# Performance work log

Measured on AMD Instinct MI355X. Metric: run time of the kernel, lower is better.

The kernel has to match this reference:

```python
import jax, jax.numpy as jnp
import numpy as np

N = 10000
E = 320000
F_IN = 256
F_PROJ = 200


def setup_inputs() -> dict:
    key = jax.random.key(0)
    ks = jax.random.split(key, 8)
    x = jax.random.normal(ks[0], (N, F_IN), dtype=jnp.float32)
    edge_attr = jax.random.uniform(ks[1], (N, N), dtype=jnp.float32)
    src = jax.random.randint(ks[2], (E,), 0, N)
    dst = jax.random.randint(ks[3], (E,), 0, N)
    # remove self loops at data-gen time (module calls remove_self_loops)
    dst = jnp.where(dst == src, (dst + 1) % N, dst)
    edge_index = jnp.stack([src, dst]).astype(jnp.int64)
    W_proj = jax.random.normal(ks[4], (F_IN, F_PROJ), dtype=jnp.float32) * 0.05
    b_proj = jnp.zeros((F_PROJ,), dtype=jnp.float32)
    W_att = jax.random.normal(ks[5], (F_PROJ, 1), dtype=jnp.float32) * 0.05
    b_att = jnp.zeros((1,), dtype=jnp.float32)
    return {"x": x, "edge_attr": edge_attr, "edge_index": edge_index,
            "W_proj": W_proj, "b_proj": b_proj, "W_att": W_att, "b_att": b_att}


def reference(x, edge_attr, edge_index, W_proj, b_proj, W_att, b_att):
    src, dst = edge_index[0], edge_index[1]
    # gather: x_j = source features, x_i = target features (PyG default flow)
    x_i = x[dst]                      # [E, F_IN]
    x_j = x[src]                      # [E, F_IN]
    p_i = x_i @ W_proj + b_proj       # [E, 200]
    p_j = x_j @ W_proj + b_proj       # [E, 200]
    alpha = jnp.abs(p_i - p_j) @ W_att + b_att   # [E, 1]
    alpha = jax.nn.relu(alpha)
    alpha = jax.nn.softmax(alpha, axis=0)        # softmax over edges
    a = alpha[:, 0]
    # write attention symmetrically into the dense edge matrix
    edge_values = edge_attr.at[src, dst].set(a).at[dst, src].set(a)
    # scatter-max aggregation of (unprojected) x_i by target index
    agg = jax.ops.segment_max(x_i, dst, num_segments=N)
    agg = jnp.where(jnp.isfinite(agg), agg, jnp.zeros((), agg.dtype))
    return agg, edge_values
```

## Files before the change

kernel.cpp:

```cpp
#include <hip/hip_runtime.h>

#define N_NODES 10000
#define E_EDGES 320000
#define F_IN    256
#define F_PROJ  200

#define N4_TOTAL 25000000L
#define S1_SPLIT 4000000L

#define K1_PROJ_BLOCKS 1250
#define K1_COPY_BLOCKS 768
#define K1_BLOCKS (K1_PROJ_BLOCKS + K1_COPY_BLOCKS)

#define K2_BLOCKS 6144
#define K2_ALPHA_BLOCKS 1536
#define K2_COPY_BLOCKS (K2_BLOCKS - K2_ALPHA_BLOCKS)
#define K2_ALPHA_WAVES (K2_ALPHA_BLOCKS * 4)
#define ALPHA_CHUNK ((E_EDGES + K2_ALPHA_WAVES - 1) / K2_ALPHA_WAVES)
#define AGG_N4 (N_NODES * F_IN / 4)
#define AGG_CHUNK ((AGG_N4 + K2_ALPHA_BLOCKS - 1) / K2_ALPHA_BLOCKS)

typedef float vfloat4 __attribute__((ext_vector_type(4)));

__device__ __forceinline__ unsigned short f32_to_bf16(float f) {
    unsigned int u = __float_as_uint(f);
    u += 0x7FFFu + ((u >> 16) & 1u);
    return (unsigned short)(u >> 16);
}
__device__ __forceinline__ float bf16_to_f32(unsigned short b) {
    return __uint_as_float(((unsigned int)b) << 16);
}

__global__ __launch_bounds__(256) void k1_proj_flags_copy(
        const float* __restrict__ x,
        const float* __restrict__ W,
        unsigned short* __restrict__ P,
        const int* __restrict__ ei,
        int* __restrict__ flags,
        const vfloat4* __restrict__ csrc,
        vfloat4* __restrict__ cdst) {
    int bid = blockIdx.x, tid = threadIdx.x;
    if (bid >= K1_PROJ_BLOCKS) {
        long i = (long)(bid - K1_PROJ_BLOCKS) * 256 + tid;
        const long stride = (long)K1_COPY_BLOCKS * 256;
        while (i + stride < S1_SPLIT) {
            vfloat4 v0 = __builtin_nontemporal_load(csrc + i);
            vfloat4 v1 = __builtin_nontemporal_load(csrc + i + stride);
            __builtin_nontemporal_store(v0, cdst + i);
            __builtin_nontemporal_store(v1, cdst + i + stride);
            i += 2 * stride;
        }
        if (i < S1_SPLIT) {
            vfloat4 v = __builtin_nontemporal_load(csrc + i);
            __builtin_nontemporal_store(v, cdst + i);
        }
        return;
    }
    int gt = bid * 256 + tid;
    flags[ei[E_EDGES + gt]] = 1;

    __shared__ float xs[8][F_IN];
    int n0 = bid * 8;
    for (int i = tid; i < 8 * F_IN / 4; i += 256)
        ((float4*)xs)[i] = ((const float4*)(x + (long)n0 * F_IN))[i];
    __syncthreads();
    int j = tid;
    if (j >= F_PROJ) return;
    float acc[8] = {0.f,0.f,0.f,0.f,0.f,0.f,0.f,0.f};
    for (int k = 0; k < F_IN; ++k) {
        float w = W[k * F_PROJ + j];
        #pragma unroll
        for (int r = 0; r < 8; ++r) acc[r] += xs[r][k] * w;
    }
    #pragma unroll
    for (int r = 0; r < 8; ++r) P[(long)(n0 + r) * F_PROJ + j] = f32_to_bf16(acc[r]);
}

__global__ __launch_bounds__(256) void k2_alpha_agg_copy(
        const int* __restrict__ ei,
        const unsigned short* __restrict__ P,
        const float* __restrict__ Watt,
        const float* __restrict__ batt,
        float* __restrict__ expalpha,
        float* __restrict__ sumbuf,
        const int* __restrict__ flags,
        const float4* __restrict__ x4,
        float4* __restrict__ agg4,
        const vfloat4* __restrict__ csrc,
        vfloat4* __restrict__ cdst) {
    int bid = blockIdx.x, tid = threadIdx.x;
    int role = bid & 3;
    if (role != 0) {
        long cid = (long)(bid >> 2) * 3 + (role - 1);
        long i = S1_SPLIT + cid * 256 + tid;
        const long stride = (long)K2_COPY_BLOCKS * 256;
        while (i + stride < N4_TOTAL) {
            vfloat4 v0 = __builtin_nontemporal_load(csrc + i);
            vfloat4 v1 = __builtin_nontemporal_load(csrc + i + stride);
            __builtin_nontemporal_store(v0, cdst + i);
            __builtin_nontemporal_store(v1, cdst + i + stride);
            i += 2 * stride;
        }
        if (i < N4_TOTAL) {
            vfloat4 v = __builtin_nontemporal_load(csrc + i);
            __builtin_nontemporal_store(v, cdst + i);
        }
        return;
    }
    __shared__ float bsum;
    if (tid == 0) bsum = 0.f;
    __syncthreads();

    int aid  = bid >> 2;
    int wid  = aid * 4 + (tid >> 6);
    int lane = tid & 63;

    float4 w4 = make_float4(0.f, 0.f, 0.f, 0.f);
    if (lane < 50) w4 = ((const float4*)Watt)[lane];
    float bias = batt[0];

    int e0 = wid * ALPHA_CHUNK;
    int e1 = min(e0 + ALPHA_CHUNK, E_EDGES);
    float lsum = 0.f;

    for (int e = e0; e < e1; ++e) {
        int s = ei[e];
        int d = ei[E_EDGES + e];
        float acc = 0.f;
        if (lane < 50) {
            uint2 us = *(const uint2*)(P + (long)s * F_PROJ + lane * 4);
            uint2 ud = *(const uint2*)(P + (long)d * F_PROJ + lane * 4);
            acc = fabsf(bf16_to_f32((unsigned short)(ud.x & 0xFFFF)) -
                        bf16_to_f32((unsigned short)(us.x & 0xFFFF))) * w4.x
                + fabsf(bf16_to_f32((unsigned short)(ud.x >> 16)) -
                        bf16_to_f32((unsigned short)(us.x >> 16))) * w4.y
                + fabsf(bf16_to_f32((unsigned short)(ud.y & 0xFFFF)) -
                        bf16_to_f32((unsigned short)(us.y & 0xFFFF))) * w4.z
                + fabsf(bf16_to_f32((unsigned short)(ud.y >> 16)) -
                        bf16_to_f32((unsigned short)(us.y >> 16))) * w4.w;
        }
        #pragma unroll
        for (int off = 32; off; off >>= 1) acc += __shfl_down(acc, off);
        if (lane == 0) {
            float alpha = fmaxf(acc + bias, 0.f);
            float ea = expf(alpha);
            expalpha[e] = ea;
            lsum += ea;
        }
    }
    if (lane == 0) atomicAdd(&bsum, lsum);
    __syncthreads();
    if (tid == 0) atomicAdd(sumbuf, bsum);

    long a0 = (long)aid * AGG_CHUNK;
    long a1 = a0 + AGG_CHUNK; if (a1 > AGG_N4) a1 = AGG_N4;
    for (long i = a0 + tid; i < a1; i += 256) {
        float4 v = x4[i];
        if (!flags[i >> 6]) v = make_float4(0.f, 0.f, 0.f, 0.f);
        agg4[i] = v;
    }
}

__global__ __launch_bounds__(256) void k3_scatter(
        const int* __restrict__ ei,
        const float* __restrict__ expalpha,
        const float* __restrict__ sumbuf,
        float* __restrict__ ev) {
    int e = blockIdx.x * 256 + threadIdx.x;
    if (e >= E_EDGES) return;
    float a = expalpha[e] / sumbuf[0];
    int s = ei[e];
    int d = ei[E_EDGES + e];
    ev[(long)s * N_NODES + d] = a;
    ev[(long)d * N_NODES + s] = a;
}

extern "C" void kernel_launch(void* const* d_in, const int* in_sizes, int n_in,
                              void* d_out, int out_size, void* d_ws, size_t ws_size,
                              hipStream_t stream) {
    (void)in_sizes; (void)n_in; (void)out_size; (void)ws_size;
    const float* x         = (const float*)d_in[0];
    const float* edge_attr = (const float*)d_in[1];
    const int*   ei        = (const int*)d_in[2];
    const float* W_proj    = (const float*)d_in[3];
    const float* W_att     = (const float*)d_in[5];
    const float* b_att     = (const float*)d_in[6];

    float* agg = (float*)d_out;
    float* ev  = (float*)d_out + (long)N_NODES * F_IN;

    char* ws = (char*)d_ws;
    unsigned short* P = (unsigned short*)(ws);
    float* expalpha   = (float*)(ws + 4000000);
    int*   flags      = (int*)  (ws + 5280000);
    float* sumbuf     = (float*)(ws + 5320000);

    hipMemsetAsync(ws + 5280000, 0, 40016, stream);

    k1_proj_flags_copy<<<K1_BLOCKS, 256, 0, stream>>>(
        x, W_proj, P, ei, flags, (const vfloat4*)edge_attr, (vfloat4*)ev);

    k2_alpha_agg_copy<<<K2_BLOCKS, 256, 0, stream>>>(
        ei, P, W_att, b_att, expalpha, sumbuf, flags,
        (const float4*)x, (float4*)agg,
        (const vfloat4*)edge_attr, (vfloat4*)ev);

    k3_scatter<<<(E_EDGES + 255) / 256, 256, 0, stream>>>(ei, expalpha, sumbuf, ev);
}
```

Baseline: 249.3 us.

## Bucket attention writes by matrix region and patch them during region copy

The dense edge-matrix copy is split into fixed 20000-float regions, spread over all three kernels with most of it in the last one. Instead of storing per-edge exp values and scattering them randomly after the copy, the alpha kernel appends (offset, fp16 exp) entries into per-region buckets using atomics. The final kernel copies each region and then patches its bucketed entries, so the scattered writes land on data that was just written. The trade-offs: buckets are capped at 384 entries and any overflow is silently dropped; values are stored in fp16; and a fallback to the old path runs only when the workspace is too small.

```diff
diff --git a/kernel.cpp b/kernel.cpp
--- a/kernel.cpp
+++ b/kernel.cpp
@@ -1,26 +1,37 @@
 #include <hip/hip_runtime.h>
+#include <hip/hip_fp16.h>
 
 #define N_NODES 10000
 #define E_EDGES 320000
 #define F_IN    256
 #define F_PROJ  200
 
-#define N4_TOTAL 25000000L
-#define S1_SPLIT 4000000L
+typedef float vfloat4 __attribute__((ext_vector_type(4)));
+
+#define REG_FLOATS 20000
+#define REG_F4     5000
+#define NREGIONS   5000
+#define CAP        384
 
 #define K1_PROJ_BLOCKS 1250
-#define K1_COPY_BLOCKS 768
-#define K1_BLOCKS (K1_PROJ_BLOCKS + K1_COPY_BLOCKS)
-
-#define K2_BLOCKS 6144
+#define K1_COPY_REGS   300
 #define K2_ALPHA_BLOCKS 1536
-#define K2_COPY_BLOCKS (K2_BLOCKS - K2_ALPHA_BLOCKS)
-#define K2_ALPHA_WAVES (K2_ALPHA_BLOCKS * 4)
+#define K2_ALPHA_WAVES  (K2_ALPHA_BLOCKS * 4)
 #define ALPHA_CHUNK ((E_EDGES + K2_ALPHA_WAVES - 1) / K2_ALPHA_WAVES)
-#define AGG_N4 (N_NODES * F_IN / 4)
-#define AGG_CHUNK ((AGG_N4 + K2_ALPHA_BLOCKS - 1) / K2_ALPHA_BLOCKS)
-
-typedef float vfloat4 __attribute__((ext_vector_type(4)));
+#define K2_COPY_REG0   300
+#define K2_COPY_REGS   600
+#define K2_AGG_BLOCKS  160
+#define AGG_N4         (N_NODES * F_IN / 4)
+#define AGG_PER_BLOCK  (AGG_N4 / K2_AGG_BLOCKS)
+#define K3_COPY_REG0   900
+#define K3_COPY_REGS   (NREGIONS - K3_COPY_REG0)
+
+#define WS_P       0L
+#define WS_FLAGS   4000000L
+#define WS_SUM     4040000L
+#define WS_COUNTS  4040016L
+#define WS_BUCKET  4060016L
+#define WS_NEED    (WS_BUCKET + (long)NREGIONS * CAP * 4)
 
 __device__ __forceinline__ unsigned short f32_to_bf16(float f) {
     unsigned int u = __float_as_uint(f);
@@ -30,6 +41,7 @@
 __device__ __forceinline__ float bf16_to_f32(unsigned short b) {
     return __uint_as_float(((unsigned int)b) << 16);
 }
+
 
 __global__ __launch_bounds__(256) void k1_proj_flags_copy(
         const float* __restrict__ x,
@@ -41,18 +53,12 @@
         vfloat4* __restrict__ cdst) {
     int bid = blockIdx.x, tid = threadIdx.x;
     if (bid >= K1_PROJ_BLOCKS) {
-        long i = (long)(bid - K1_PROJ_BLOCKS) * 256 + tid;
-        const long stride = (long)K1_COPY_BLOCKS * 256;
-        while (i + stride < S1_SPLIT) {
-            vfloat4 v0 = __builtin_nontemporal_load(csrc + i);
-            vfloat4 v1 = __builtin_nontemporal_load(csrc + i + stride);
-            __builtin_nontemporal_store(v0, cdst + i);
-            __builtin_nontemporal_store(v1, cdst + i + stride);
-            i += 2 * stride;
-        }
-        if (i < S1_SPLIT) {
-            vfloat4 v = __builtin_nontemporal_load(csrc + i);
-            __builtin_nontemporal_store(v, cdst + i);
+        long r = bid - K1_PROJ_BLOCKS;
+        const vfloat4* s = csrc + r * REG_F4;
+        vfloat4*       d = cdst + r * REG_F4;
+        for (int i = tid; i < REG_F4; i += 256) {
+            vfloat4 v = __builtin_nontemporal_load(s + i);
+            __builtin_nontemporal_store(v, d + i);
         }
         return;
     }
@@ -76,32 +82,177 @@
     for (int r = 0; r < 8; ++r) P[(long)(n0 + r) * F_PROJ + j] = f32_to_bf16(acc[r]);
 }
 
-__global__ __launch_bounds__(256) void k2_alpha_agg_copy(
+__global__ __launch_bounds__(256) void k2_alpha_copy_agg(
         const int* __restrict__ ei,
         const unsigned short* __restrict__ P,
         const float* __restrict__ Watt,
         const float* __restrict__ batt,
-        float* __restrict__ expalpha,
         float* __restrict__ sumbuf,
+        unsigned int* __restrict__ counts,
+        unsigned int* __restrict__ bucket,
         const int* __restrict__ flags,
         const float4* __restrict__ x4,
         float4* __restrict__ agg4,
         const vfloat4* __restrict__ csrc,
         vfloat4* __restrict__ cdst) {
     int bid = blockIdx.x, tid = threadIdx.x;
+    if (bid < K2_ALPHA_BLOCKS) {
+        __shared__ float bsum;
+        if (tid == 0) bsum = 0.f;
+        __syncthreads();
+        int wid  = bid * 4 + (tid >> 6);
+        int lane = tid & 63;
+        float4 w4 = make_float4(0.f, 0.f, 0.f, 0.f);
+        if (lane < 50) w4 = ((const float4*)Watt)[lane];
+        float bias = batt[0];
+        int e0 = wid * ALPHA_CHUNK;
+        int e1 = min(e0 + ALPHA_CHUNK, E_EDGES);
+        float lsum = 0.f;
+        for (int e = e0; e < e1; ++e) {
+            int s = ei[e];
+            int d = ei[E_EDGES + e];
+            float acc = 0.f;
+            if (lane < 50) {
+                uint2 us = *(const uint2*)(P + (long)s * F_PROJ + lane * 4);
+                uint2 ud = *(const uint2*)(P + (long)d * F_PROJ + lane * 4);
+                acc = fabsf(bf16_to_f32((unsigned short)(ud.x & 0xFFFF)) -
+                            bf16_to_f32((unsigned short)(us.x & 0xFFFF))) * w4.x
+                    + fabsf(bf16_to_f32((unsigned short)(ud.x >> 16)) -
+                            bf16_to_f32((unsigned short)(us.x >> 16))) * w4.y
+                    + fabsf(bf16_to_f32((unsigned short)(ud.y & 0xFFFF)) -
+                            bf16_to_f32((unsigned short)(us.y & 0xFFFF))) * w4.z
+                    + fabsf(bf16_to_f32((unsigned short)(ud.y >> 16)) -
+                            bf16_to_f32((unsigned short)(us.y >> 16))) * w4.w;
+            }
+            #pragma unroll
+            for (int off = 32; off; off >>= 1) acc += __shfl_xor(acc, off);
+            float alpha = fmaxf(acc + bias, 0.f);
+            float ea = expf(alpha);
+            if (lane < 2) {
+                unsigned int li = (lane == 0)
+                    ? (unsigned int)s * 10000u + (unsigned int)d
+                    : (unsigned int)d * 10000u + (unsigned int)s;
+                unsigned int r  = li / 20000u;
+                unsigned int p  = li - r * 20000u;
+                unsigned short h = __half_as_ushort(__float2half(ea));
+                unsigned int idx = atomicAdd(&counts[r], 1u);
+                if (idx < CAP) bucket[(long)r * CAP + idx] = (p << 16) | h;
+                if (lane == 0) lsum += ea;
+            }
+        }
+        if (lane == 0) atomicAdd(&bsum, lsum);
+        __syncthreads();
+        if (tid == 0) atomicAdd(sumbuf, bsum);
+        return;
+    }
+    int b2 = bid - K2_ALPHA_BLOCKS;
+    if (b2 < K2_COPY_REGS) {
+        long r = K2_COPY_REG0 + b2;
+        const vfloat4* s = csrc + r * REG_F4;
+        vfloat4*       d = cdst + r * REG_F4;
+        for (int i = tid; i < REG_F4; i += 256) {
+            vfloat4 v = __builtin_nontemporal_load(s + i);
+            __builtin_nontemporal_store(v, d + i);
+        }
+        return;
+    }
+    long base = (long)(b2 - K2_COPY_REGS) * AGG_PER_BLOCK;
+    for (int i = tid; i < AGG_PER_BLOCK; i += 256) {
+        long i4 = base + i;
+        float4 v = x4[i4];
+        if (!flags[i4 >> 6]) v = make_float4(0.f, 0.f, 0.f, 0.f);
+        agg4[i4] = v;
+    }
+}
+
+__global__ __launch_bounds__(256) void k3_copy_patch(
+        const unsigned int* __restrict__ counts,
+        const unsigned int* __restrict__ bucket,
+        const float* __restrict__ sumbuf,
+        const vfloat4* __restrict__ csrc,
+        vfloat4* __restrict__ cdst,
+        float* __restrict__ ev) {
+    int bid = blockIdx.x, tid = threadIdx.x;
+    int r;
+    if (bid < K3_COPY_REGS) {
+        r = K3_COPY_REG0 + bid;
+        const vfloat4* s = csrc + (long)r * REG_F4;
+        vfloat4*       d = cdst + (long)r * REG_F4;
+        for (int i = tid; i < REG_F4; i += 256) d[i] = s[i];
+        __syncthreads();
+    } else {
+        r = bid - K3_COPY_REGS;
+    }
+    unsigned int cnt = counts[r];
+    if (cnt > CAP) cnt = CAP;
+    float inv = 1.0f / sumbuf[0];
+    long base = (long)r * REG_FLOATS;
+    for (unsigned int i = tid; i < cnt; i += 256) {
+        unsigned int en = bucket[(long)r * CAP + i];
+        float a = __half2float(__ushort_as_half((unsigned short)(en & 0xFFFFu))) * inv;
+        ev[base + (en >> 16)] = a;
+    }
+}
+
+#define N4_TOTAL 25000000L
+#define S1_SPLIT 4000000L
+#define FB1_PROJ_BLOCKS 1250
+#define FB1_COPY_BLOCKS 768
+#define FB2_BLOCKS 6144
+#define FB2_ALPHA_BLOCKS 1536
+#define FB2_COPY_BLOCKS (FB2_BLOCKS - FB2_ALPHA_BLOCKS)
+#define FB2_ALPHA_WAVES (FB2_ALPHA_BLOCKS * 4)
+#define FB_ALPHA_CHUNK ((E_EDGES + FB2_ALPHA_WAVES - 1) / FB2_ALPHA_WAVES)
+#define FB_AGG_CHUNK ((AGG_N4 + FB2_ALPHA_BLOCKS - 1) / FB2_ALPHA_BLOCKS)
+
+__global__ __launch_bounds__(256) void fb1_proj_flags_copy(
+        const float* __restrict__ x, const float* __restrict__ W,
+        unsigned short* __restrict__ P, const int* __restrict__ ei,
+        int* __restrict__ flags,
+        const vfloat4* __restrict__ csrc, vfloat4* __restrict__ cdst) {
+    int bid = blockIdx.x, tid = threadIdx.x;
+    if (bid >= FB1_PROJ_BLOCKS) {
+        long i = (long)(bid - FB1_PROJ_BLOCKS) * 256 + tid;
+        const long stride = (long)FB1_COPY_BLOCKS * 256;
+        for (; i < S1_SPLIT; i += stride) {
+            vfloat4 v = __builtin_nontemporal_load(csrc + i);
+            __builtin_nontemporal_store(v, cdst + i);
+        }
+        return;
+    }
+    int gt = bid * 256 + tid;
+    flags[ei[E_EDGES + gt]] = 1;
+    __shared__ float xs[8][F_IN];
+    int n0 = bid * 8;
+    for (int i = tid; i < 8 * F_IN / 4; i += 256)
+        ((float4*)xs)[i] = ((const float4*)(x + (long)n0 * F_IN))[i];
+    __syncthreads();
+    int j = tid;
+    if (j >= F_PROJ) return;
+    float acc[8] = {0.f,0.f,0.f,0.f,0.f,0.f,0.f,0.f};
+    for (int k = 0; k < F_IN; ++k) {
+        float w = W[k * F_PROJ + j];
+        #pragma unroll
+        for (int r = 0; r < 8; ++r) acc[r] += xs[r][k] * w;
+    }
+    #pragma unroll
+    for (int r = 0; r < 8; ++r) P[(long)(n0 + r) * F_PROJ + j] = f32_to_bf16(acc[r]);
+}
+
+__global__ __launch_bounds__(256) void fb2_alpha_agg_copy(
+        const int* __restrict__ ei, const unsigned short* __restrict__ P,
+        const float* __restrict__ Watt, const float* __restrict__ batt,
+        float* __restrict__ expalpha, float* __restrict__ sumbuf,
+        const int* __restrict__ flags, const float4* __restrict__ x4,
+        float4* __restrict__ agg4,
+        const vfloat4* __restrict__ csrc, vfloat4* __restrict__ cdst) {
+    int bid = blockIdx.x, tid = threadIdx.x;
     int role = bid & 3;
     if (role != 0) {
         long cid = (long)(bid >> 2) * 3 + (role - 1);
         long i = S1_SPLIT + cid * 256 + tid;
-        const long stride = (long)K2_COPY_BLOCKS * 256;
-        while (i + stride < N4_TOTAL) {
-            vfloat4 v0 = __builtin_nontemporal_load(csrc + i);
-            vfloat4 v1 = __builtin_nontemporal_load(csrc + i + stride);
-            __builtin_nontemporal_store(v0, cdst + i);
-            __builtin_nontemporal_store(v1, cdst + i + stride);
-            i += 2 * stride;
-        }
-        if (i < N4_TOTAL) {
+        const long stride = (long)FB2_COPY_BLOCKS * 256;
+        for (; i < N4_TOTAL; i += stride) {
             vfloat4 v = __builtin_nontemporal_load(csrc + i);
             __builtin_nontemporal_store(v, cdst + i);
         }
@@ -110,22 +261,14 @@
     __shared__ float bsum;
     if (tid == 0) bsum = 0.f;
     __syncthreads();
-
-    int aid  = bid >> 2;
-    int wid  = aid * 4 + (tid >> 6);
-    int lane = tid & 63;
-
+    int aid = bid >> 2, wid = aid * 4 + (tid >> 6), lane = tid & 63;
     float4 w4 = make_float4(0.f, 0.f, 0.f, 0.f);
     if (lane < 50) w4 = ((const float4*)Watt)[lane];
     float bias = batt[0];
-
-    int e0 = wid * ALPHA_CHUNK;
-    int e1 = min(e0 + ALPHA_CHUNK, E_EDGES);
+    int e0 = wid * FB_ALPHA_CHUNK, e1 = min(e0 + FB_ALPHA_CHUNK, E_EDGES);
     float lsum = 0.f;
-
     for (int e = e0; e < e1; ++e) {
-        int s = ei[e];
-        int d = ei[E_EDGES + e];
+        int s = ei[e], d = ei[E_EDGES + e];
         float acc = 0.f;
         if (lane < 50) {
             uint2 us = *(const uint2*)(P + (long)s * F_PROJ + lane * 4);
@@ -142,8 +285,7 @@
         #pragma unroll
         for (int off = 32; off; off >>= 1) acc += __shfl_down(acc, off);
         if (lane == 0) {
-            float alpha = fmaxf(acc + bias, 0.f);
-            float ea = expf(alpha);
+            float ea = expf(fmaxf(acc + bias, 0.f));
             expalpha[e] = ea;
             lsum += ea;
         }
@@ -151,9 +293,8 @@
     if (lane == 0) atomicAdd(&bsum, lsum);
     __syncthreads();
     if (tid == 0) atomicAdd(sumbuf, bsum);
-
-    long a0 = (long)aid * AGG_CHUNK;
-    long a1 = a0 + AGG_CHUNK; if (a1 > AGG_N4) a1 = AGG_N4;
+    long a0 = (long)aid * FB_AGG_CHUNK;
+    long a1 = a0 + FB_AGG_CHUNK; if (a1 > AGG_N4) a1 = AGG_N4;
     for (long i = a0 + tid; i < a1; i += 256) {
         float4 v = x4[i];
         if (!flags[i >> 6]) v = make_float4(0.f, 0.f, 0.f, 0.f);
@@ -161,16 +302,13 @@
     }
 }
 
-__global__ __launch_bounds__(256) void k3_scatter(
-        const int* __restrict__ ei,
-        const float* __restrict__ expalpha,
-        const float* __restrict__ sumbuf,
-        float* __restrict__ ev) {
+__global__ __launch_bounds__(256) void fb3_scatter(
+        const int* __restrict__ ei, const float* __restrict__ expalpha,
+        const float* __restrict__ sumbuf, float* __restrict__ ev) {
     int e = blockIdx.x * 256 + threadIdx.x;
     if (e >= E_EDGES) return;
     float a = expalpha[e] / sumbuf[0];
-    int s = ei[e];
-    int d = ei[E_EDGES + e];
+    int s = ei[e], d = ei[E_EDGES + e];
     ev[(long)s * N_NODES + d] = a;
     ev[(long)d * N_NODES + s] = a;
 }
@@ -178,7 +316,7 @@
 extern "C" void kernel_launch(void* const* d_in, const int* in_sizes, int n_in,
                               void* d_out, int out_size, void* d_ws, size_t ws_size,
                               hipStream_t stream) {
-    (void)in_sizes; (void)n_in; (void)out_size; (void)ws_size;
+    (void)in_sizes; (void)n_in; (void)out_size;
     const float* x         = (const float*)d_in[0];
     const float* edge_attr = (const float*)d_in[1];
     const int*   ei        = (const int*)d_in[2];
@@ -188,22 +326,45 @@
 
     float* agg = (float*)d_out;
     float* ev  = (float*)d_out + (long)N_NODES * F_IN;
-
     char* ws = (char*)d_ws;
-    unsigned short* P = (unsigned short*)(ws);
-    float* expalpha   = (float*)(ws + 4000000);
-    int*   flags      = (int*)  (ws + 5280000);
-    float* sumbuf     = (float*)(ws + 5320000);
-
-    hipMemsetAsync(ws + 5280000, 0, 40016, stream);
-
-    k1_proj_flags_copy<<<K1_BLOCKS, 256, 0, stream>>>(
-        x, W_proj, P, ei, flags, (const vfloat4*)edge_attr, (vfloat4*)ev);
-
-    k2_alpha_agg_copy<<<K2_BLOCKS, 256, 0, stream>>>(
-        ei, P, W_att, b_att, expalpha, sumbuf, flags,
-        (const float4*)x, (float4*)agg,
-        (const vfloat4*)edge_attr, (vfloat4*)ev);
-
-    k3_scatter<<<(E_EDGES + 255) / 256, 256, 0, stream>>>(ei, expalpha, sumbuf, ev);
-}
+
+    if (ws_size >= (size_t)WS_NEED) {
+        unsigned short* P   = (unsigned short*)(ws + WS_P);
+        int*   flags        = (int*)(ws + WS_FLAGS);
+        float* sumbuf       = (float*)(ws + WS_SUM);
+        unsigned int* cnts  = (unsigned int*)(ws + WS_COUNTS);
+        unsigned int* bkt   = (unsigned int*)(ws + WS_BUCKET);
+
+        hipMemsetAsync(ws + WS_FLAGS, 0, WS_BUCKET - WS_FLAGS, stream);
+
+        k1_proj_flags_copy<<<K1_PROJ_BLOCKS + K1_COPY_REGS, 256, 0, stream>>>(
+            x, W_proj, P, ei, flags, (const vfloat4*)edge_attr, (vfloat4*)ev);
+
+        k2_alpha_copy_agg<<<K2_ALPHA_BLOCKS + K2_COPY_REGS + K2_AGG_BLOCKS, 256, 0,
+                            stream>>>(
+            ei, P, W_att, b_att, sumbuf, cnts, bkt, flags,
+            (const float4*)x, (float4*)agg,
+            (const vfloat4*)edge_attr, (vfloat4*)ev);
+
+        k3_copy_patch<<<NREGIONS, 256, 0, stream>>>(
+            cnts, bkt, sumbuf, (const vfloat4*)edge_attr, (vfloat4*)ev, ev);
+    } else {
+        unsigned short* P = (unsigned short*)(ws);
+        float* expalpha   = (float*)(ws + 4000000);
+        int*   flags      = (int*)(ws + 5280000);
+        float* sumbuf     = (float*)(ws + 5320000);
+
+        hipMemsetAsync(ws + 5280000, 0, 40016, stream);
+
+        fb1_proj_flags_copy<<<FB1_PROJ_BLOCKS + FB1_COPY_BLOCKS, 256, 0, stream>>>(
+            x, W_proj, P, ei, flags, (const vfloat4*)edge_attr, (vfloat4*)ev);
+
+        fb2_alpha_agg_copy<<<FB2_BLOCKS, 256, 0, stream>>>(
+            ei, P, W_att, b_att, expalpha, sumbuf, flags,
+            (const float4*)x, (float4*)agg,
+            (const vfloat4*)edge_attr, (vfloat4*)ev);
+
+        fb3_scatter<<<(E_EDGES + 255) / 256, 256, 0, stream>>>(
+            ei, expalpha, sumbuf, ev);
+    }
+}
```

Result: slower. 321.6 us (+29.0%).

## Split bulk edge_attr copy out of alpha kernel into separate copy kernel

Applied to the files above, without the earlier changes.

The alpha/aggregation kernel no longer interleaves copy blocks. The bulk of the dense edge_attr-to-output copy now runs in its own kernel, which uses plain loads and stores instead of nontemporal ones. Alpha work is regrouped into 2048 blocks of 40 edges per wave, and aggregation gets 160 dedicated blocks. The aim is to balance the alpha gather and the streaming copy better, at the cost of losing their overlap and adding one kernel launch.

```diff
diff --git a/kernel.cpp b/kernel.cpp
--- a/kernel.cpp
+++ b/kernel.cpp
@@ -5,22 +5,24 @@
 #define F_IN    256
 #define F_PROJ  200
 
+typedef float vfloat4 __attribute__((ext_vector_type(4)));
+
 #define N4_TOTAL 25000000L
 #define S1_SPLIT 4000000L
 
 #define K1_PROJ_BLOCKS 1250
 #define K1_COPY_BLOCKS 768
-#define K1_BLOCKS (K1_PROJ_BLOCKS + K1_COPY_BLOCKS)
+#define A_BLOCKS    2048
+#define A_CHUNK     40
+#define AGG_BLOCKS  160
+#define AGG_N4      (N_NODES * F_IN / 4)
+#define AGG_PER_BLK (AGG_N4 / AGG_BLOCKS)
+#define K3_BLOCKS   4096
 
-#define K2_BLOCKS 6144
-#define K2_ALPHA_BLOCKS 1536
-#define K2_COPY_BLOCKS (K2_BLOCKS - K2_ALPHA_BLOCKS)
-#define K2_ALPHA_WAVES (K2_ALPHA_BLOCKS * 4)
-#define ALPHA_CHUNK ((E_EDGES + K2_ALPHA_WAVES - 1) / K2_ALPHA_WAVES)
-#define AGG_N4 (N_NODES * F_IN / 4)
-#define AGG_CHUNK ((AGG_N4 + K2_ALPHA_BLOCKS - 1) / K2_ALPHA_BLOCKS)
-
-typedef float vfloat4 __attribute__((ext_vector_type(4)));
+#define WS_P      0L
+#define WS_EXP    4000000L
+#define WS_FLAGS  5280000L
+#define WS_SUM    5320000L
 
 __device__ __forceinline__ unsigned short f32_to_bf16(float f) {
     unsigned int u = __float_as_uint(f);
@@ -32,25 +34,15 @@
 }
 
 __global__ __launch_bounds__(256) void k1_proj_flags_copy(
-        const float* __restrict__ x,
-        const float* __restrict__ W,
-        unsigned short* __restrict__ P,
-        const int* __restrict__ ei,
+        const float* __restrict__ x, const float* __restrict__ W,
+        unsigned short* __restrict__ P, const int* __restrict__ ei,
         int* __restrict__ flags,
-        const vfloat4* __restrict__ csrc,
-        vfloat4* __restrict__ cdst) {
+        const vfloat4* __restrict__ csrc, vfloat4* __restrict__ cdst) {
     int bid = blockIdx.x, tid = threadIdx.x;
     if (bid >= K1_PROJ_BLOCKS) {
         long i = (long)(bid - K1_PROJ_BLOCKS) * 256 + tid;
         const long stride = (long)K1_COPY_BLOCKS * 256;
-        while (i + stride < S1_SPLIT) {
-            vfloat4 v0 = __builtin_nontemporal_load(csrc + i);
-            vfloat4 v1 = __builtin_nontemporal_load(csrc + i + stride);
-            __builtin_nontemporal_store(v0, cdst + i);
-            __builtin_nontemporal_store(v1, cdst + i + stride);
-            i += 2 * stride;
-        }
-        if (i < S1_SPLIT) {
+        for (; i < S1_SPLIT; i += stride) {
             vfloat4 v = __builtin_nontemporal_load(csrc + i);
             __builtin_nontemporal_store(v, cdst + i);
         }
@@ -76,101 +68,83 @@
     for (int r = 0; r < 8; ++r) P[(long)(n0 + r) * F_PROJ + j] = f32_to_bf16(acc[r]);
 }
 
-__global__ __launch_bounds__(256) void k2_alpha_agg_copy(
-        const int* __restrict__ ei,
-        const unsigned short* __restrict__ P,
-        const float* __restrict__ Watt,
-        const float* __restrict__ batt,
-        float* __restrict__ expalpha,
-        float* __restrict__ sumbuf,
-        const int* __restrict__ flags,
-        const float4* __restrict__ x4,
-        float4* __restrict__ agg4,
-        const vfloat4* __restrict__ csrc,
-        vfloat4* __restrict__ cdst) {
+__global__ __launch_bounds__(256) void k2_alpha_agg(
+        const int* __restrict__ ei, const unsigned short* __restrict__ P,
+        const float* __restrict__ Watt, const float* __restrict__ batt,
+        float* __restrict__ expalpha, float* __restrict__ sumbuf,
+        const int* __restrict__ flags, const float4* __restrict__ x4,
+        float4* __restrict__ agg4) {
     int bid = blockIdx.x, tid = threadIdx.x;
-    int role = bid & 3;
-    if (role != 0) {
-        long cid = (long)(bid >> 2) * 3 + (role - 1);
-        long i = S1_SPLIT + cid * 256 + tid;
-        const long stride = (long)K2_COPY_BLOCKS * 256;
-        while (i + stride < N4_TOTAL) {
-            vfloat4 v0 = __builtin_nontemporal_load(csrc + i);
-            vfloat4 v1 = __builtin_nontemporal_load(csrc + i + stride);
-            __builtin_nontemporal_store(v0, cdst + i);
-            __builtin_nontemporal_store(v1, cdst + i + stride);
-            i += 2 * stride;
+    if (bid < A_BLOCKS) {
+        __shared__ float bsum;
+        if (tid == 0) bsum = 0.f;
+        __syncthreads();
+        int wid  = bid * 4 + (tid >> 6);
+        int lane = tid & 63;
+        float4 w4 = make_float4(0.f, 0.f, 0.f, 0.f);
+        if (lane < 50) w4 = ((const float4*)Watt)[lane];
+        float bias = batt[0];
+        int e0 = wid * A_CHUNK;
+        int e1 = min(e0 + A_CHUNK, E_EDGES);
+        float lsum = 0.f;
+        for (int e = e0; e < e1; ++e) {
+            int s = ei[e];
+            int d = ei[E_EDGES + e];
+            float acc = 0.f;
+            if (lane < 50) {
+                uint2 us = *(const uint2*)(P + (long)s * F_PROJ + lane * 4);
+                uint2 ud = *(const uint2*)(P + (long)d * F_PROJ + lane * 4);
+                acc = fabsf(bf16_to_f32((unsigned short)(ud.x & 0xFFFF)) -
+                            bf16_to_f32((unsigned short)(us.x & 0xFFFF))) * w4.x
+                    + fabsf(bf16_to_f32((unsigned short)(ud.x >> 16)) -
+                            bf16_to_f32((unsigned short)(us.x >> 16))) * w4.y
+                    + fabsf(bf16_to_f32((unsigned short)(ud.y & 0xFFFF)) -
+                            bf16_to_f32((unsigned short)(us.y & 0xFFFF))) * w4.z
+                    + fabsf(bf16_to_f32((unsigned short)(ud.y >> 16)) -
+                            bf16_to_f32((unsigned short)(us.y >> 16))) * w4.w;
+            }
+            #pragma unroll
+            for (int off = 32; off; off >>= 1) acc += __shfl_down(acc, off);
+            if (lane == 0) {
+                float ea = expf(fmaxf(acc + bias, 0.f));
+                expalpha[e] = ea;
+                lsum += ea;
+            }
         }
-        if (i < N4_TOTAL) {
-            vfloat4 v = __builtin_nontemporal_load(csrc + i);
-            __builtin_nontemporal_store(v, cdst + i);
-        }
+        if (lane == 0) atomicAdd(&bsum, lsum);
+        __syncthreads();
+        if (tid == 0) atomicAdd(sumbuf, bsum);
         return;
     }
-    __shared__ float bsum;
-    if (tid == 0) bsum = 0.f;
-    __syncthreads();
-
-    int aid  = bid >> 2;
-    int wid  = aid * 4 + (tid >> 6);
-    int lane = tid & 63;
-
-    float4 w4 = make_float4(0.f, 0.f, 0.f, 0.f);
-    if (lane < 50) w4 = ((const float4*)Watt)[lane];
-    float bias = batt[0];
-
-    int e0 = wid * ALPHA_CHUNK;
-    int e1 = min(e0 + ALPHA_CHUNK, E_EDGES);
-    float lsum = 0.f;
-
-    for (int e = e0; e < e1; ++e) {
-        int s = ei[e];
-        int d = ei[E_EDGES + e];
-        float acc = 0.f;
-        if (lane < 50) {
-            uint2 us = *(const uint2*)(P + (long)s * F_PROJ + lane * 4);
-            uint2 ud = *(const uint2*)(P + (long)d * F_PROJ + lane * 4);
-            acc = fabsf(bf16_to_f32((unsigned short)(ud.x & 0xFFFF)) -
-                        bf16_to_f32((unsigned short)(us.x & 0xFFFF))) * w4.x
-                + fabsf(bf16_to_f32((unsigned short)(ud.x >> 16)) -
-                        bf16_to_f32((unsigned short)(us.x >> 16))) * w4.y
-                + fabsf(bf16_to_f32((unsigned short)(ud.y & 0xFFFF)) -
-                        bf16_to_f32((unsigned short)(us.y & 0xFFFF))) * w4.z
-                + fabsf(bf16_to_f32((unsigned short)(ud.y >> 16)) -
-                        bf16_to_f32((unsigned short)(us.y >> 16))) * w4.w;
-        }
-        #pragma unroll
-        for (int off = 32; off; off >>= 1) acc += __shfl_down(acc, off);
-        if (lane == 0) {
-            float alpha = fmaxf(acc + bias, 0.f);
-            float ea = expf(alpha);
-            expalpha[e] = ea;
-            lsum += ea;
-        }
-    }
-    if (lane == 0) atomicAdd(&bsum, lsum);
-    __syncthreads();
-    if (tid == 0) atomicAdd(sumbuf, bsum);
-
-    long a0 = (long)aid * AGG_CHUNK;
-    long a1 = a0 + AGG_CHUNK; if (a1 > AGG_N4) a1 = AGG_N4;
-    for (long i = a0 + tid; i < a1; i += 256) {
-        float4 v = x4[i];
-        if (!flags[i >> 6]) v = make_float4(0.f, 0.f, 0.f, 0.f);
-        agg4[i] = v;
+    long base = (long)(bid - A_BLOCKS) * AGG_PER_BLK;
+    for (int i = tid; i < AGG_PER_BLK; i += 256) {
+        long i4 = base + i;
+        float4 v = x4[i4];
+        if (!flags[i4 >> 6]) v = make_float4(0.f, 0.f, 0.f, 0.f);
+        agg4[i4] = v;
     }
 }
 
-__global__ __launch_bounds__(256) void k3_scatter(
-        const int* __restrict__ ei,
-        const float* __restrict__ expalpha,
-        const float* __restrict__ sumbuf,
-        float* __restrict__ ev) {
+__global__ __launch_bounds__(256) void k3_copy(
+        const vfloat4* __restrict__ src, vfloat4* __restrict__ dst) {
+    long i = S1_SPLIT + (long)blockIdx.x * 256 + threadIdx.x;
+    const long stride = (long)K3_BLOCKS * 256;
+    for (; i + stride < N4_TOTAL; i += 2 * stride) {
+        vfloat4 a = src[i];
+        vfloat4 b = src[i + stride];
+        dst[i] = a;
+        dst[i + stride] = b;
+    }
+    if (i < N4_TOTAL) dst[i] = src[i];
+}
+
+__global__ __launch_bounds__(256) void k4_scatter(
+        const int* __restrict__ ei, const float* __restrict__ expalpha,
+        const float* __restrict__ sumbuf, float* __restrict__ ev) {
     int e = blockIdx.x * 256 + threadIdx.x;
     if (e >= E_EDGES) return;
     float a = expalpha[e] / sumbuf[0];
-    int s = ei[e];
-    int d = ei[E_EDGES + e];
+    int s = ei[e], d = ei[E_EDGES + e];
     ev[(long)s * N_NODES + d] = a;
     ev[(long)d * N_NODES + s] = a;
 }
@@ -188,22 +162,25 @@
 
     float* agg = (float*)d_out;
     float* ev  = (float*)d_out + (long)N_NODES * F_IN;
+    char* ws = (char*)d_ws;
 
-    char* ws = (char*)d_ws;
-    unsigned short* P = (unsigned short*)(ws);
-    float* expalpha   = (float*)(ws + 4000000);
-    int*   flags      = (int*)  (ws + 5280000);
-    float* sumbuf     = (float*)(ws + 5320000);
+    unsigned short* P = (unsigned short*)(ws + WS_P);
+    float* expalpha   = (float*)(ws + WS_EXP);
+    int*   flags      = (int*)(ws + WS_FLAGS);
+    float* sumbuf     = (float*)(ws + WS_SUM);
 
-    hipMemsetAsync(ws + 5280000, 0, 40016, stream);
+    hipMemsetAsync(ws + WS_FLAGS, 0, 40016, stream);
 
-    k1_proj_flags_copy<<<K1_BLOCKS, 256, 0, stream>>>(
+    k1_proj_flags_copy<<<K1_PROJ_BLOCKS + K1_COPY_BLOCKS, 256, 0, stream>>>(
         x, W_proj, P, ei, flags, (const vfloat4*)edge_attr, (vfloat4*)ev);
 
-    k2_alpha_agg_copy<<<K2_BLOCKS, 256, 0, stream>>>(
+    k2_alpha_agg<<<A_BLOCKS + AGG_BLOCKS, 256, 0, stream>>>(
         ei, P, W_att, b_att, expalpha, sumbuf, flags,
-        (const float4*)x, (float4*)agg,
+        (const float4*)x, (float4*)agg);
+
+    k3_copy<<<K3_BLOCKS, 256, 0, stream>>>(
         (const vfloat4*)edge_attr, (vfloat4*)ev);
 
-    k3_scatter<<<(E_EDGES + 255) / 256, 256, 0, stream>>>(ei, expalpha, sumbuf, ev);
+    k4_scatter<<<(E_EDGES + 255) / 256, 256, 0, stream>>>(
+        ei, expalpha, sumbuf, ev);
 }
```

After: 294.6 us. 1.18x slower.
